# Optimization experiments

Measured on AMD Instinct MI355X. Metric: run time of the kernel, lower is better.

Reference implementation:

```python
import jax, jax.numpy as jnp
import numpy as np

THRESHOLD = 0.5
EPS = 1e-6

def cxcywh_to_xyxy(b):
    return jnp.concatenate([b[..., :2] - b[..., 2:] / 2, b[..., :2] + b[..., 2:] / 2], axis=-1)

def xyxy_to_cxcywh(b):
    return jnp.concatenate([(b[..., :2] + b[..., 2:]) / 2, b[..., 2:] - b[..., :2]], axis=-1)

def iou_matrix(a, b, eps):
    # a: [P,4] xyxy, b: [O,4] xyxy -> [P,O]
    lb = jnp.maximum(a[:, None, :2], b[None, :, :2])
    ub = jnp.minimum(a[:, None, 2:], b[None, :, 2:])
    wh = jnp.clip(ub - lb, 0.0)
    inter = wh[..., 0] * wh[..., 1]
    area_a = (a[:, 2] - a[:, 0]) * (a[:, 3] - a[:, 1])
    area_b = (b[:, 2] - b[:, 0]) * (b[:, 3] - b[:, 1])
    union = area_a[:, None] + area_b[None, :] - inter
    return inter / (union + eps)

def match_single(priors_xyxy, t_xyxy, t_labels):
    # SSD-style matching (stand-in for Calculate_bbox_target_classes)
    n_obj = t_xyxy.shape[0]
    iou = iou_matrix(priors_xyxy, t_xyxy, EPS)          # [P,O]
    best_obj_iou = jnp.max(iou, axis=1)                 # [P]
    best_obj = jnp.argmax(iou, axis=1)                  # [P]
    best_prior = jnp.argmax(iou, axis=0)                # [O] force-match each object
    best_obj = best_obj.at[best_prior].set(jnp.arange(n_obj))
    best_obj_iou = best_obj_iou.at[best_prior].set(1.0)
    labels = t_labels[best_obj]                          # [P]
    labels = jnp.where(best_obj_iou < THRESHOLD, 0, labels)
    locs = xyxy_to_cxcywh(t_xyxy[best_obj])              # [P,4] cxcywh
    return labels, locs

def setup_inputs() -> dict:
    key = jax.random.key(0)
    k1, k2, k3, k4, k5, k6, k7 = jax.random.split(key, 7)
    B, P, C, O = 64, 8732, 81, 32
    # predictions: cxcywh-ish boxes in [0,1]
    pl_xy = jax.random.uniform(k1, (B, P, 2))
    pl_wh = jax.random.uniform(k2, (B, P, 2)) * 0.25 + 0.02
    predictlocs = jnp.concatenate([pl_xy, pl_wh], axis=-1)
    predictcls = jax.random.normal(k3, (B, P, C))
    pr_xy = jax.random.uniform(k4, (P, 2))
    pr_wh = jax.random.uniform(k5, (P, 2)) * 0.25 + 0.02
    prior_bboxes = jnp.concatenate([pr_xy, pr_wh], axis=-1)
    tb_xy = jax.random.uniform(k6, (B, O, 2)) * 0.8
    tb_wh = jax.random.uniform(k7, (B, O, 2)) * 0.2 + 0.02
    target_bboxes = jnp.concatenate([tb_xy, tb_wh], axis=-1)  # xywh
    target_labels = jax.random.randint(jax.random.fold_in(key, 99), (B, O), 1, C)
    return {"predictlocs": predictlocs, "predictcls": predictcls,
            "prior_bboxes": prior_bboxes, "target_bboxes": target_bboxes,
            "target_labels": target_labels}

def _iou_loss_masked(pred_cxcywh, tgt_cxcywh, pos_mask):
    tp = cxcywh_to_xyxy(tgt_cxcywh)
    bp = cxcywh_to_xyxy(pred_cxcywh)
    lb = jnp.maximum(tp[..., :2], bp[..., :2])
    ub = jnp.minimum(tp[..., 2:], bp[..., 2:])
    wh = jnp.clip(ub - lb, 0.0)
    inter = wh[..., 0] * wh[..., 1]
    area_b = (bp[..., 2] - bp[..., 0]) * (bp[..., 3] - bp[..., 1])
    area_t = (tp[..., 2] - tp[..., 0]) * (tp[..., 3] - tp[..., 1])
    union = area_t + area_b - inter
    v = 1.0 - inter / (union + EPS)
    n_pos = jnp.sum(pos_mask)
    return jnp.sum(jnp.where(pos_mask, v, 0.0)) / n_pos

def reference(predictlocs, predictcls, prior_bboxes, target_bboxes, target_labels):
    n_classes = predictcls.shape[2]
    # xywh -> xyxy, as in original forward
    t_xyxy = jnp.concatenate([target_bboxes[..., :2],
                              target_bboxes[..., :2] + target_bboxes[..., 2:]], axis=-1)
    priors_xyxy = cxcywh_to_xyxy(prior_bboxes)
    true_classes, true_locs = jax.vmap(match_single, in_axes=(None, 0, 0))(
        priors_xyxy, t_xyxy, target_labels)      # [B,P], [B,P,4]
    pos = true_classes != 0                       # [B,P]
    n_pos = jnp.sum(pos).astype(predictlocs.dtype)
    # IoU loss over positives (mean over positives)
    iou_loss = _iou_loss_masked(predictlocs, true_locs, pos)
    # L1 loss (mean over all elements of selected [Npos,4])
    l1 = jnp.abs(predictlocs - true_locs)
    loc_loss = jnp.sum(jnp.where(pos[..., None], l1, 0.0)) / (n_pos * 4.0)
    # CrossEntropy over all priors (mean)
    logp = jax.nn.log_softmax(predictcls.reshape(-1, n_classes), axis=-1)
    cross_loss = -jnp.mean(jnp.take_along_axis(
        logp, true_classes.reshape(-1, 1), axis=-1))
    return loc_loss, cross_loss, iou_loss
```

## Files before the change

kernel.cpp:

```cpp
#include <hip/hip_runtime.h>
#include <hip/hip_bf16.h>

#define NB 64
#define NP 8732
#define NO 32
#define NC 81
#define NROWS (NB * NP)
#define ITERS (NROWS / 16)
#define LGRID 2048


__device__ __forceinline__ float ldT(const float* p, size_t i) { return p[i]; }
__device__ __forceinline__ float ldT(const unsigned short* p, size_t i) {
    return __uint_as_float((unsigned)p[i] << 16);
}
__device__ __forceinline__ float4 ld4(const float* p, size_t i) {
    return *(const float4*)(p + i);
}
__device__ __forceinline__ float4 ld4(const unsigned short* p, size_t i) {
    ushort4 u = *(const ushort4*)(p + i);
    return make_float4(__uint_as_float((unsigned)u.x << 16),
                       __uint_as_float((unsigned)u.y << 16),
                       __uint_as_float((unsigned)u.z << 16),
                       __uint_as_float((unsigned)u.w << 16));
}

__global__ void init_kernel(const void* __restrict__ prior,
                            unsigned long long* __restrict__ bestPrior,
                            float* __restrict__ accum, int* __restrict__ flag) {
    int i = threadIdx.x;
    for (int j = i; j < NB * NO; j += blockDim.x) bestPrior[j] = 0ull;
    if (i < 4) accum[i] = 0.0f;
    if (i < 64) {
        const unsigned short* pb = (const unsigned short*)prior;
        float v = __uint_as_float((unsigned)pb[i] << 16);
        unsigned long long bad = __ballot(!(fabsf(v) <= 8.0f));
        if (i == 0) *flag = (__popcll(bad) >= 8) ? 1 : 0;
    }
}

template <typename T>
__device__ __forceinline__ void match_body(
        const T* __restrict__ prior, const T* __restrict__ tb,
        unsigned long long* __restrict__ bestPrior) {
    const int b   = blockIdx.y;
    const int o   = threadIdx.x & 31;
    const int seg = threadIdx.x >> 5;
    const int p0  = blockIdx.x * 256 + seg * 32;

    float4 t = ld4(tb, ((size_t)(b * NO + o)) * 4);
    float tx0 = t.x, ty0 = t.y, tx1 = t.x + t.z, ty1 = t.y + t.w, ta = t.z * t.w;

    float bi = -1.0f;
    int bp = 0;
    for (int j = 0; j < 32; ++j) {
        int p = p0 + j;
        if (p >= NP) break;
        float4 pr = ld4(prior, (size_t)p * 4);
        float px0 = pr.x - pr.z * 0.5f, py0 = pr.y - pr.w * 0.5f;
        float px1 = pr.x + pr.z * 0.5f, py1 = pr.y + pr.w * 0.5f;
        float pa = (px1 - px0) * (py1 - py0);
        float lbx = fmaxf(px0, tx0), lby = fmaxf(py0, ty0);
        float ubx = fminf(px1, tx1), uby = fminf(py1, ty1);
        float ww = fmaxf(ubx - lbx, 0.0f), hh = fmaxf(uby - lby, 0.0f);
        float inter = ww * hh;
        float iou = inter / (pa + ta - inter + 1e-6f);
        if (iou > bi) { bi = iou; bp = p; }
    }
    if (bi >= 0.0f) {
        unsigned long long packed =
            (((unsigned long long)__float_as_uint(bi)) << 32) | (~(unsigned)bp);
        atomicMax(&bestPrior[b * NO + o], packed);
    }
}

__global__ __launch_bounds__(256) void match_kernel(
        const void* __restrict__ prior, const void* __restrict__ tb,
        unsigned long long* __restrict__ bestPrior, const int* __restrict__ flag) {
    if (*flag)
        match_body<float>((const float*)prior, (const float*)tb, bestPrior);
    else
        match_body<unsigned short>((const unsigned short*)prior,
                                   (const unsigned short*)tb, bestPrior);
}

template <typename T>
__device__ void loss_impl(
        const T* __restrict__ plocs, const T* __restrict__ pcls,
        const T* __restrict__ prior, const T* __restrict__ tb,
        const int* __restrict__ tlab,
        const unsigned long long* __restrict__ bestPrior,
        float* __restrict__ accum) {
    const int tid = threadIdx.x;
    const int lane = tid & 63;
    const int wv = tid >> 6;
    const int q = lane & 15;
    const int g = lane >> 4;

    float c_sum = 0.f, l1_sum = 0.f, iou_sum = 0.f, np_sum = 0.f;

    for (int it = blockIdx.x; it < ITERS; it += gridDim.x) {
        const int row = it * 16 + wv * 4 + g;
        const int b = row / NP;
        const int p = row - b * NP;

        float4 pr = ld4(prior, (size_t)p * 4);
        float px0 = pr.x - pr.z * 0.5f, py0 = pr.y - pr.w * 0.5f;
        float px1 = pr.x + pr.z * 0.5f, py1 = pr.y + pr.w * 0.5f;
        float pa = (px1 - px0) * (py1 - py0);

        float bi; int bo;
        {
            float4 t = ld4(tb, ((size_t)(b * NO + q)) * 4);
            float lbx = fmaxf(px0, t.x),       lby = fmaxf(py0, t.y);
            float ubx = fminf(px1, t.x + t.z), uby = fminf(py1, t.y + t.w);
            float ww = fmaxf(ubx - lbx, 0.f), hh = fmaxf(uby - lby, 0.f);
            float inter = ww * hh;
            bi = inter / (pa + t.z * t.w - inter + 1e-6f);
            bo = q;
        }
        {
            float4 t = ld4(tb, ((size_t)(b * NO + q + 16)) * 4);
            float lbx = fmaxf(px0, t.x),       lby = fmaxf(py0, t.y);
            float ubx = fminf(px1, t.x + t.z), uby = fminf(py1, t.y + t.w);
            float ww = fmaxf(ubx - lbx, 0.f), hh = fmaxf(uby - lby, 0.f);
            float inter = ww * hh;
            float iou2 = inter / (pa + t.z * t.w - inter + 1e-6f);
            if (iou2 > bi) { bi = iou2; bo = q + 16; }
        }
        #pragma unroll
        for (int d = 1; d < 16; d <<= 1) {
            float obi = __shfl_xor(bi, d);
            int   obo = __shfl_xor(bo, d);
            if (obi > bi || (obi == bi && obo < bo)) { bi = obi; bo = obo; }
        }
        int fo = -1;
        if (~(unsigned)(bestPrior[b * NO + q] & 0xffffffffull) == (unsigned)p)
            fo = q;
        if (~(unsigned)(bestPrior[b * NO + q + 16] & 0xffffffffull) == (unsigned)p)
            fo = q + 16;
        #pragma unroll
        for (int d = 1; d < 16; d <<= 1) fo = max(fo, __shfl_xor(fo, d));
        if (fo >= 0) { bo = fo; bi = 1.0f; }

        int lab = tlab[b * NO + bo];
        if (bi < 0.5f) lab = 0;

        const T* xr = pcls + (size_t)row * NC;
        float v[5];
        #pragma unroll
        for (int j = 0; j < 5; ++j) v[j] = ldT(xr, q + 16 * j);
        float v80 = (q == 0) ? ldT(xr, 80) : -1e30f;
        float m = fmaxf(fmaxf(fmaxf(v[0], v[1]), fmaxf(v[2], v[3])),
                        fmaxf(v[4], v80));
        #pragma unroll
        for (int d = 1; d < 16; d <<= 1) m = fmaxf(m, __shfl_xor(m, d));
        float s = __expf(v[0] - m) + __expf(v[1] - m) + __expf(v[2] - m)
                + __expf(v[3] - m) + __expf(v[4] - m) + __expf(v80 - m);
        #pragma unroll
        for (int d = 1; d < 16; d <<= 1) s += __shfl_xor(s, d);

        if (q == 0) {
            float lse = m + __logf(s);
            float xl = ldT(xr, lab);
            c_sum += lse - xl;
            if (lab != 0) {
                np_sum += 1.0f;
                float4 t = ld4(tb, ((size_t)(b * NO + bo)) * 4);
                float x0 = t.x, y0 = t.y, x1 = t.x + t.z, y1 = t.y + t.w;
                float tcx = (x0 + x1) * 0.5f, tcy = (y0 + y1) * 0.5f;
                float4 qv = ld4(plocs, (size_t)row * 4);
                l1_sum += fabsf(qv.x - tcx) + fabsf(qv.y - tcy)
                        + fabsf(qv.z - t.z) + fabsf(qv.w - t.w);
                float qX0 = qv.x - qv.z * 0.5f, qY0 = qv.y - qv.w * 0.5f;
                float qX1 = qv.x + qv.z * 0.5f, qY1 = qv.y + qv.w * 0.5f;
                float lbx = fmaxf(x0, qX0), lby = fmaxf(y0, qY0);
                float ubx = fminf(x1, qX1), uby = fminf(y1, qY1);
                float iw = fmaxf(ubx - lbx, 0.f), ih = fmaxf(uby - lby, 0.f);
                float inter = iw * ih;
                float areaq = (qX1 - qX0) * (qY1 - qY0);
                float areat = (x1 - x0) * (y1 - y0);
                iou_sum += 1.0f - inter / (areat + areaq - inter + 1e-6f);
            }
        }
    }

    #pragma unroll
    for (int d = 1; d < 64; d <<= 1) {
        c_sum   += __shfl_xor(c_sum, d);
        l1_sum  += __shfl_xor(l1_sum, d);
        iou_sum += __shfl_xor(iou_sum, d);
        np_sum  += __shfl_xor(np_sum, d);
    }
    __shared__ float red[4][4];
    if (lane == 0) { red[wv][0] = c_sum; red[wv][1] = l1_sum;
                     red[wv][2] = iou_sum; red[wv][3] = np_sum; }
    __syncthreads();
    if (tid == 0) {
        float a0 = 0, a1 = 0, a2 = 0, a3 = 0;
        for (int k = 0; k < 4; ++k) { a0 += red[k][0]; a1 += red[k][1];
                                      a2 += red[k][2]; a3 += red[k][3]; }
        atomicAdd(&accum[0], a0);
        atomicAdd(&accum[1], a1);
        atomicAdd(&accum[2], a2);
        atomicAdd(&accum[3], a3);
    }
}

__global__ __launch_bounds__(256) void loss_kernel(
        const void* __restrict__ plocs, const void* __restrict__ pcls,
        const void* __restrict__ prior, const void* __restrict__ tb,
        const int* __restrict__ tlab,
        const unsigned long long* __restrict__ bestPrior,
        const int* __restrict__ flag, float* __restrict__ accum) {
    if (*flag)
        loss_impl<float>((const float*)plocs, (const float*)pcls,
                         (const float*)prior, (const float*)tb,
                         tlab, bestPrior, accum);
    else
        loss_impl<unsigned short>((const unsigned short*)plocs,
                                  (const unsigned short*)pcls,
                                  (const unsigned short*)prior,
                                  (const unsigned short*)tb,
                                  tlab, bestPrior, accum);
}

__global__ void finalize_kernel(const float* __restrict__ accum,
                                const int* __restrict__ flag, void* __restrict__ out) {
    if (threadIdx.x == 0) {
        float cross = accum[0] / (float)NROWS;
        float npos = accum[3];
        float loc = accum[1] / (npos * 4.0f);
        float iou = accum[2] / npos;
        if (*flag) {
            float* o = (float*)out;
            o[0] = loc; o[1] = cross; o[2] = iou;
        } else {
            __hip_bfloat16* o = (__hip_bfloat16*)out;
            o[0] = __float2bfloat16(loc);
            o[1] = __float2bfloat16(cross);
            o[2] = __float2bfloat16(iou);
        }
    }
}

extern "C" void kernel_launch(void* const* d_in, const int* in_sizes, int n_in,
                              void* d_out, int out_size, void* d_ws, size_t ws_size,
                              hipStream_t stream) {
    const void* plocs = d_in[0];
    const void* pcls  = d_in[1];
    const void* prior = d_in[2];
    const void* tb    = d_in[3];
    const int*  tlab  = (const int*)d_in[4];

    char* w = (char*)d_ws;
    unsigned long long* bestPrior = (unsigned long long*)w;
    float* accum = (float*)(w + 16384);
    int*   flag  = (int*)(w + 16400);

    hipLaunchKernelGGL(init_kernel, dim3(1), dim3(256), 0, stream,
                       prior, bestPrior, accum, flag);

    dim3 gA((NP + 255) / 256, NB);
    hipLaunchKernelGGL(match_kernel, gA, dim3(256), 0, stream,
                       prior, tb, bestPrior, flag);

    hipLaunchKernelGGL(loss_kernel, dim3(LGRID), dim3(256), 0, stream,
                       plocs, pcls, prior, tb, tlab, bestPrior, flag, accum);

    hipLaunchKernelGGL(finalize_kernel, dim3(1), dim3(64), 0, stream,
                       accum, flag, d_out);
}
```

Measured before the change: 397.3 us.

## Split loss kernel into per-row matching prep and a dual-row cross-entropy pass

Splits the fused loss kernel in two. A prep kernel gives each thread one prior row, stages the batch's target boxes, labels and forced matches in shared memory, and does the 32-object argmax serially. It writes a byte label per row and accumulates the L1, IoU and positive-count sums. A separate cross-entropy kernel reads the byte labels and processes two rows per wave group per iteration, so more class-logit loads are in flight at once. This removes the 16-lane shuffle argmax from the bandwidth-bound softmax path, at the cost of an extra launch and a small label buffer round-trip through memory.

```diff
diff --git a/kernel.cpp b/kernel.cpp
--- a/kernel.cpp
+++ b/kernel.cpp
@@ -6,8 +6,9 @@
 #define NO 32
 #define NC 81
 #define NROWS (NB * NP)
+#define PBLK 2183
 #define ITERS (NROWS / 16)
-#define LGRID 2048
+#define CGRID 2048
 
 
 __device__ __forceinline__ float ldT(const float* p, size_t i) { return p[i]; }
@@ -85,144 +86,189 @@
 }
 
 template <typename T>
-__device__ void loss_impl(
-        const T* __restrict__ plocs, const T* __restrict__ pcls,
-        const T* __restrict__ prior, const T* __restrict__ tb,
-        const int* __restrict__ tlab,
+__device__ void prep_impl(
+        const T* __restrict__ plocs, const T* __restrict__ prior,
+        const T* __restrict__ tb, const int* __restrict__ tlab,
         const unsigned long long* __restrict__ bestPrior,
-        float* __restrict__ accum) {
+        unsigned char* __restrict__ lab8, float* __restrict__ accum) {
+    __shared__ float4 s_box[2][NO];
+    __shared__ float  s_area[2][NO];
+    __shared__ int    s_lab[2][NO];
+    __shared__ unsigned s_forced[2][NO];
+    __shared__ float red[4][3];
+
+    const int tid = threadIdx.x;
+    const int lane = tid & 63;
+    const int wv = tid >> 6;
+    const int row = blockIdx.x * 256 + tid;
+    const int b = row / NP;
+    const int p = row - b * NP;
+    const int b0 = (blockIdx.x * 256) / NP;
+
+    if (tid < 64) {
+        int bb = tid >> 5, o = tid & 31;
+        int bq = b0 + bb;
+        if (bq < NB) {
+            float4 t = ld4(tb, ((size_t)(bq * NO + o)) * 4);
+            s_box[bb][o] = make_float4(t.x, t.y, t.x + t.z, t.y + t.w);
+            s_area[bb][o] = t.z * t.w;
+            s_lab[bb][o] = tlab[bq * NO + o];
+            s_forced[bb][o] = ~(unsigned)(bestPrior[bq * NO + o] & 0xffffffffull);
+        }
+    }
+    __syncthreads();
+
+    const int bb = b - b0;
+    float4 pr = ld4(prior, (size_t)p * 4);
+    float px0 = pr.x - pr.z * 0.5f, py0 = pr.y - pr.w * 0.5f;
+    float px1 = pr.x + pr.z * 0.5f, py1 = pr.y + pr.w * 0.5f;
+    float pa = (px1 - px0) * (py1 - py0);
+
+    float bi = -1.0f;
+    int bo = 0, fo = -1;
+    for (int o = 0; o < NO; ++o) {
+        float4 t = s_box[bb][o];
+        float lbx = fmaxf(px0, t.x), lby = fmaxf(py0, t.y);
+        float ubx = fminf(px1, t.z), uby = fminf(py1, t.w);
+        float ww = fmaxf(ubx - lbx, 0.0f), hh = fmaxf(uby - lby, 0.0f);
+        float inter = ww * hh;
+        float iou = inter / (pa + s_area[bb][o] - inter + 1e-6f);
+        if (iou > bi) { bi = iou; bo = o; }
+        if (s_forced[bb][o] == (unsigned)p) fo = o;
+    }
+    if (fo >= 0) { bo = fo; bi = 1.0f; }
+
+    int lab = s_lab[bb][bo];
+    if (bi < 0.5f) lab = 0;
+    lab8[row] = (unsigned char)lab;
+
+    float l1_sum = 0.f, iou_sum = 0.f, np_sum = 0.f;
+    if (lab != 0) {
+        np_sum = 1.0f;
+        float4 t = s_box[bb][bo];
+        float x0 = t.x, y0 = t.y, x1 = t.z, y1 = t.w;
+        float tw = x1 - x0, th = y1 - y0;
+        float4 traw = ld4(tb, ((size_t)(b * NO + bo)) * 4);
+        float tcx = (x0 + x1) * 0.5f, tcy = (y0 + y1) * 0.5f;
+        float4 qv = ld4(plocs, (size_t)row * 4);
+        l1_sum = fabsf(qv.x - tcx) + fabsf(qv.y - tcy)
+               + fabsf(qv.z - traw.z) + fabsf(qv.w - traw.w);
+        float qX0 = qv.x - qv.z * 0.5f, qY0 = qv.y - qv.w * 0.5f;
+        float qX1 = qv.x + qv.z * 0.5f, qY1 = qv.y + qv.w * 0.5f;
+        float lbx = fmaxf(x0, qX0), lby = fmaxf(y0, qY0);
+        float ubx = fminf(x1, qX1), uby = fminf(y1, qY1);
+        float iw = fmaxf(ubx - lbx, 0.f), ih = fmaxf(uby - lby, 0.f);
+        float inter = iw * ih;
+        float areaq = (qX1 - qX0) * (qY1 - qY0);
+        float areat = (x1 - x0) * (y1 - y0);
+        iou_sum = 1.0f - inter / (areat + areaq - inter + 1e-6f);
+        (void)tw; (void)th;
+    }
+
+    #pragma unroll
+    for (int d = 1; d < 64; d <<= 1) {
+        l1_sum  += __shfl_xor(l1_sum, d);
+        iou_sum += __shfl_xor(iou_sum, d);
+        np_sum  += __shfl_xor(np_sum, d);
+    }
+    if (lane == 0) { red[wv][0] = l1_sum; red[wv][1] = iou_sum; red[wv][2] = np_sum; }
+    __syncthreads();
+    if (tid == 0) {
+        float a1 = 0, a2 = 0, a3 = 0;
+        for (int k = 0; k < 4; ++k) { a1 += red[k][0]; a2 += red[k][1]; a3 += red[k][2]; }
+        atomicAdd(&accum[1], a1);
+        atomicAdd(&accum[2], a2);
+        atomicAdd(&accum[3], a3);
+    }
+}
+
+__global__ __launch_bounds__(256) void prep_kernel(
+        const void* __restrict__ plocs, const void* __restrict__ prior,
+        const void* __restrict__ tb, const int* __restrict__ tlab,
+        const unsigned long long* __restrict__ bestPrior,
+        const int* __restrict__ flag,
+        unsigned char* __restrict__ lab8, float* __restrict__ accum) {
+    if (*flag)
+        prep_impl<float>((const float*)plocs, (const float*)prior,
+                         (const float*)tb, tlab, bestPrior, lab8, accum);
+    else
+        prep_impl<unsigned short>((const unsigned short*)plocs,
+                                  (const unsigned short*)prior,
+                                  (const unsigned short*)tb,
+                                  tlab, bestPrior, lab8, accum);
+}
+
+template <typename T>
+__device__ void ce_impl(const T* __restrict__ pcls,
+                        const unsigned char* __restrict__ lab8,
+                        float* __restrict__ accum) {
     const int tid = threadIdx.x;
     const int lane = tid & 63;
     const int wv = tid >> 6;
     const int q = lane & 15;
-    const int g = lane >> 4;
-
-    float c_sum = 0.f, l1_sum = 0.f, iou_sum = 0.f, np_sum = 0.f;
-
-    for (int it = blockIdx.x; it < ITERS; it += gridDim.x) {
-        const int row = it * 16 + wv * 4 + g;
-        const int b = row / NP;
-        const int p = row - b * NP;
-
-        float4 pr = ld4(prior, (size_t)p * 4);
-        float px0 = pr.x - pr.z * 0.5f, py0 = pr.y - pr.w * 0.5f;
-        float px1 = pr.x + pr.z * 0.5f, py1 = pr.y + pr.w * 0.5f;
-        float pa = (px1 - px0) * (py1 - py0);
-
-        float bi; int bo;
-        {
-            float4 t = ld4(tb, ((size_t)(b * NO + q)) * 4);
-            float lbx = fmaxf(px0, t.x),       lby = fmaxf(py0, t.y);
-            float ubx = fminf(px1, t.x + t.z), uby = fminf(py1, t.y + t.w);
-            float ww = fmaxf(ubx - lbx, 0.f), hh = fmaxf(uby - lby, 0.f);
-            float inter = ww * hh;
-            bi = inter / (pa + t.z * t.w - inter + 1e-6f);
-            bo = q;
-        }
-        {
-            float4 t = ld4(tb, ((size_t)(b * NO + q + 16)) * 4);
-            float lbx = fmaxf(px0, t.x),       lby = fmaxf(py0, t.y);
-            float ubx = fminf(px1, t.x + t.z), uby = fminf(py1, t.y + t.w);
-            float ww = fmaxf(ubx - lbx, 0.f), hh = fmaxf(uby - lby, 0.f);
-            float inter = ww * hh;
-            float iou2 = inter / (pa + t.z * t.w - inter + 1e-6f);
-            if (iou2 > bi) { bi = iou2; bo = q + 16; }
-        }
+
+    float c_sum = 0.f;
+
+    for (int it0 = blockIdx.x; it0 < ITERS; it0 += 2 * CGRID) {
+        int it1 = it0 + CGRID;
+        bool hasB = (it1 < ITERS);
+        int rowA = it0 * 16 + wv * 4 + (lane >> 4);
+        int rowB = hasB ? (it1 * 16 + wv * 4 + (lane >> 4)) : rowA;
+
+        int labA = lab8[rowA];
+        int labB = lab8[rowB];
+        const T* xrA = pcls + (size_t)rowA * NC;
+        const T* xrB = pcls + (size_t)rowB * NC;
+
+        float vA[5], vB[5];
+        #pragma unroll
+        for (int j = 0; j < 5; ++j) { vA[j] = ldT(xrA, q + 16 * j);
+                                      vB[j] = ldT(xrB, q + 16 * j); }
+        float v80A = (q == 0) ? ldT(xrA, 80) : -1e30f;
+        float v80B = (q == 0) ? ldT(xrB, 80) : -1e30f;
+        float xlA = (q == 0) ? ldT(xrA, labA) : 0.f;
+        float xlB = (q == 0) ? ldT(xrB, labB) : 0.f;
+
+        float mA = fmaxf(fmaxf(fmaxf(vA[0], vA[1]), fmaxf(vA[2], vA[3])),
+                         fmaxf(vA[4], v80A));
+        float mB = fmaxf(fmaxf(fmaxf(vB[0], vB[1]), fmaxf(vB[2], vB[3])),
+                         fmaxf(vB[4], v80B));
         #pragma unroll
         for (int d = 1; d < 16; d <<= 1) {
-            float obi = __shfl_xor(bi, d);
-            int   obo = __shfl_xor(bo, d);
-            if (obi > bi || (obi == bi && obo < bo)) { bi = obi; bo = obo; }
-        }
-        int fo = -1;
-        if (~(unsigned)(bestPrior[b * NO + q] & 0xffffffffull) == (unsigned)p)
-            fo = q;
-        if (~(unsigned)(bestPrior[b * NO + q + 16] & 0xffffffffull) == (unsigned)p)
-            fo = q + 16;
+            mA = fmaxf(mA, __shfl_xor(mA, d));
+            mB = fmaxf(mB, __shfl_xor(mB, d));
+        }
+        float sA = __expf(vA[0] - mA) + __expf(vA[1] - mA) + __expf(vA[2] - mA)
+                 + __expf(vA[3] - mA) + __expf(vA[4] - mA) + __expf(v80A - mA);
+        float sB = __expf(vB[0] - mB) + __expf(vB[1] - mB) + __expf(vB[2] - mB)
+                 + __expf(vB[3] - mB) + __expf(vB[4] - mB) + __expf(v80B - mB);
         #pragma unroll
-        for (int d = 1; d < 16; d <<= 1) fo = max(fo, __shfl_xor(fo, d));
-        if (fo >= 0) { bo = fo; bi = 1.0f; }
-
-        int lab = tlab[b * NO + bo];
-        if (bi < 0.5f) lab = 0;
-
-        const T* xr = pcls + (size_t)row * NC;
-        float v[5];
-        #pragma unroll
-        for (int j = 0; j < 5; ++j) v[j] = ldT(xr, q + 16 * j);
-        float v80 = (q == 0) ? ldT(xr, 80) : -1e30f;
-        float m = fmaxf(fmaxf(fmaxf(v[0], v[1]), fmaxf(v[2], v[3])),
-                        fmaxf(v[4], v80));
-        #pragma unroll
-        for (int d = 1; d < 16; d <<= 1) m = fmaxf(m, __shfl_xor(m, d));
-        float s = __expf(v[0] - m) + __expf(v[1] - m) + __expf(v[2] - m)
-                + __expf(v[3] - m) + __expf(v[4] - m) + __expf(v80 - m);
-        #pragma unroll
-        for (int d = 1; d < 16; d <<= 1) s += __shfl_xor(s, d);
-
+        for (int d = 1; d < 16; d <<= 1) {
+            sA += __shfl_xor(sA, d);
+            sB += __shfl_xor(sB, d);
+        }
         if (q == 0) {
-            float lse = m + __logf(s);
-            float xl = ldT(xr, lab);
-            c_sum += lse - xl;
-            if (lab != 0) {
-                np_sum += 1.0f;
-                float4 t = ld4(tb, ((size_t)(b * NO + bo)) * 4);
-                float x0 = t.x, y0 = t.y, x1 = t.x + t.z, y1 = t.y + t.w;
-                float tcx = (x0 + x1) * 0.5f, tcy = (y0 + y1) * 0.5f;
-                float4 qv = ld4(plocs, (size_t)row * 4);
-                l1_sum += fabsf(qv.x - tcx) + fabsf(qv.y - tcy)
-                        + fabsf(qv.z - t.z) + fabsf(qv.w - t.w);
-                float qX0 = qv.x - qv.z * 0.5f, qY0 = qv.y - qv.w * 0.5f;
-                float qX1 = qv.x + qv.z * 0.5f, qY1 = qv.y + qv.w * 0.5f;
-                float lbx = fmaxf(x0, qX0), lby = fmaxf(y0, qY0);
-                float ubx = fminf(x1, qX1), uby = fminf(y1, qY1);
-                float iw = fmaxf(ubx - lbx, 0.f), ih = fmaxf(uby - lby, 0.f);
-                float inter = iw * ih;
-                float areaq = (qX1 - qX0) * (qY1 - qY0);
-                float areat = (x1 - x0) * (y1 - y0);
-                iou_sum += 1.0f - inter / (areat + areaq - inter + 1e-6f);
-            }
+            c_sum += (mA + __logf(sA)) - xlA;
+            if (hasB) c_sum += (mB + __logf(sB)) - xlB;
         }
     }
 
     #pragma unroll
-    for (int d = 1; d < 64; d <<= 1) {
-        c_sum   += __shfl_xor(c_sum, d);
-        l1_sum  += __shfl_xor(l1_sum, d);
-        iou_sum += __shfl_xor(iou_sum, d);
-        np_sum  += __shfl_xor(np_sum, d);
-    }
-    __shared__ float red[4][4];
-    if (lane == 0) { red[wv][0] = c_sum; red[wv][1] = l1_sum;
-                     red[wv][2] = iou_sum; red[wv][3] = np_sum; }
+    for (int d = 1; d < 64; d <<= 1) c_sum += __shfl_xor(c_sum, d);
+    __shared__ float red[4];
+    if (lane == 0) red[wv] = c_sum;
     __syncthreads();
-    if (tid == 0) {
-        float a0 = 0, a1 = 0, a2 = 0, a3 = 0;
-        for (int k = 0; k < 4; ++k) { a0 += red[k][0]; a1 += red[k][1];
-                                      a2 += red[k][2]; a3 += red[k][3]; }
-        atomicAdd(&accum[0], a0);
-        atomicAdd(&accum[1], a1);
-        atomicAdd(&accum[2], a2);
-        atomicAdd(&accum[3], a3);
-    }
-}
-
-__global__ __launch_bounds__(256) void loss_kernel(
-        const void* __restrict__ plocs, const void* __restrict__ pcls,
-        const void* __restrict__ prior, const void* __restrict__ tb,
-        const int* __restrict__ tlab,
-        const unsigned long long* __restrict__ bestPrior,
+    if (tid == 0)
+        atomicAdd(&accum[0], red[0] + red[1] + red[2] + red[3]);
+}
+
+__global__ __launch_bounds__(256) void ce_kernel(
+        const void* __restrict__ pcls, const unsigned char* __restrict__ lab8,
         const int* __restrict__ flag, float* __restrict__ accum) {
     if (*flag)
-        loss_impl<float>((const float*)plocs, (const float*)pcls,
-                         (const float*)prior, (const float*)tb,
-                         tlab, bestPrior, accum);
+        ce_impl<float>((const float*)pcls, lab8, accum);
     else
-        loss_impl<unsigned short>((const unsigned short*)plocs,
-                                  (const unsigned short*)pcls,
-                                  (const unsigned short*)prior,
-                                  (const unsigned short*)tb,
-                                  tlab, bestPrior, accum);
+        ce_impl<unsigned short>((const unsigned short*)pcls, lab8, accum);
 }
 
 __global__ void finalize_kernel(const float* __restrict__ accum,
@@ -257,6 +303,7 @@
     unsigned long long* bestPrior = (unsigned long long*)w;
     float* accum = (float*)(w + 16384);
     int*   flag  = (int*)(w + 16400);
+    unsigned char* lab8 = (unsigned char*)(w + 16408);
 
     hipLaunchKernelGGL(init_kernel, dim3(1), dim3(256), 0, stream,
                        prior, bestPrior, accum, flag);
@@ -265,8 +312,11 @@
     hipLaunchKernelGGL(match_kernel, gA, dim3(256), 0, stream,
                        prior, tb, bestPrior, flag);
 
-    hipLaunchKernelGGL(loss_kernel, dim3(LGRID), dim3(256), 0, stream,
-                       plocs, pcls, prior, tb, tlab, bestPrior, flag, accum);
+    hipLaunchKernelGGL(prep_kernel, dim3(PBLK), dim3(256), 0, stream,
+                       plocs, prior, tb, tlab, bestPrior, flag, lab8, accum);
+
+    hipLaunchKernelGGL(ce_kernel, dim3(CGRID), dim3(256), 0, stream,
+                       pcls, lab8, flag, accum);
 
     hipLaunchKernelGGL(finalize_kernel, dim3(1), dim3(64), 0, stream,
                        accum, flag, d_out);
```

After: 390.7 us. No clear change (-1.7%).
